# Performance work log

Hardware: AMD Instinct MI355X
Metric: run time of the kernel (lower is better)

## Reference

```python
import jax, jax.numpy as jnp
import numpy as np

TAU = 2.0        # LIF membrane time constant
VTH = 1.0        # firing threshold
ALPHA = 2.0      # ATan surrogate sharpness (spikingjelly default)
EPS = 1e-5       # LayerNorm eps


@jax.custom_vjp
def spike(x):
    # Heaviside forward, ATan surrogate backward (spikingjelly surrogate.ATan)
    return (x >= 0).astype(x.dtype)

def _spike_fwd(x):
    return (x >= 0).astype(x.dtype), x

def _spike_bwd(x, g):
    return (g * (ALPHA / 2.0) / (1.0 + (jnp.pi / 2.0 * ALPHA * x) ** 2),)

spike.defvjp(_spike_fwd, _spike_bwd)


def lif(x_tbd):
    """Multi-step LIF neuron, decay_input=True, hard reset v_reset=0, detach_reset=True.
    x_tbd: [T, B, D] -> spikes [T, B, D]."""
    def step(v, x):
        v = v + (x - v) / TAU                       # leaky integrate
        s = spike(v - VTH)                          # fire
        v = v * (1.0 - jax.lax.stop_gradient(s))    # detached hard reset to 0
        return v, s
    v0 = jnp.zeros(x_tbd.shape[1:], x_tbd.dtype)
    _, s = jax.lax.scan(step, v0, x_tbd)
    return s


def layernorm(x, g, b):
    m = x.mean(-1, keepdims=True)
    v = ((x - m) ** 2).mean(-1, keepdims=True)
    return (x - m) * jax.lax.rsqrt(v + EPS) * g + b


def setup_inputs() -> dict:
    key = jax.random.key(0)
    ks = jax.random.split(key, 8)
    B, T, IN, H0, D, HD, DEPTH = 64, 2048, 4, 64, 128, 256, 4
    def w(k, shape, fan_in):
        return jax.random.normal(k, shape, jnp.float32) * (1.0 / np.sqrt(fan_in))
    return {
        "hist_feat": jax.random.normal(ks[0], (B, T, IN), jnp.float32),
        # projector params
        "pw1": w(ks[1], (IN, H0), IN), "pb1": jnp.zeros((H0,), jnp.float32),
        "pw2": w(ks[2], (H0, D), H0), "pb2": jnp.zeros((D,), jnp.float32),
        # stacked block params [DEPTH, ...]
        "fc1_w": w(ks[3], (DEPTH, D, HD), D), "fc1_b": jnp.zeros((DEPTH, HD), jnp.float32),
        "n1_g": jnp.ones((DEPTH, HD), jnp.float32), "n1_b": jnp.zeros((DEPTH, HD), jnp.float32),
        "fc2_w": w(ks[4], (DEPTH, HD, D), HD), "fc2_b": jnp.zeros((DEPTH, D), jnp.float32),
        "n2_g": jnp.ones((DEPTH, D), jnp.float32), "n2_b": jnp.zeros((DEPTH, D), jnp.float32),
    }


def reference(hist_feat, pw1, pb1, pw2, pb2, fc1_w, fc1_b, n1_g, n1_b,
              fc2_w, fc2_b, n2_g, n2_b):
    # SpikeInputProjector: Linear -> exact GELU -> Linear
    x = jax.nn.gelu(hist_feat @ pw1 + pb1, approximate=False) @ pw2 + pb2  # [B,T,D]
    depth = fc1_w.shape[0]
    for i in range(depth):  # small fixed structural loop over blocks
        r = x
        h = layernorm(x @ fc1_w[i] + fc1_b[i], n1_g[i], n1_b[i])   # [B,T,HD]
        h = lif(h.swapaxes(0, 1)).swapaxes(0, 1)                    # LIF over time
        h = layernorm(h @ fc2_w[i] + fc2_b[i], n2_g[i], n2_b[i])   # [B,T,D]
        h = lif(h.swapaxes(0, 1)).swapaxes(0, 1)
        x = r + h
    return x[:, -1]  # pooling='last', mask=None
```

## Files before the change

### kernel.cpp

```cpp
#include <hip/hip_runtime.h>
#include <math.h>

#define NB   64
#define TT   2048
#define TW   64
#define T0   (TT - TW)
#define NR   (NB * TW)

typedef float v2f __attribute__((ext_vector_type(2)));

__device__ __forceinline__ float gelu_exact(float x) {
    return 0.5f * x * (1.0f + erff(x * 0.7071067811865476f));
}

#define XT_O   0
#define WB0_O  4096
#define WB1_O  20480
#define V1_O   36864
#define V2_O   37120
#define LB_TOT 37248

__global__ void __launch_bounds__(512) fused_kernel(
    const float* __restrict__ hist,
    const float* __restrict__ pw1, const float* __restrict__ pb1,
    const float* __restrict__ pw2, const float* __restrict__ pb2,
    const float* __restrict__ fc1w, const float* __restrict__ fc1b,
    const float* __restrict__ n1g,  const float* __restrict__ n1b,
    const float* __restrict__ fc2w, const float* __restrict__ fc2b,
    const float* __restrict__ n2g,  const float* __restrict__ n2b,
    float* __restrict__ v1buf, float* __restrict__ v2buf,
    int* __restrict__ flg1, int* __restrict__ flg2,
    float* __restrict__ out)
{
    __shared__ __align__(16) float LB[LB_TOT];
    __shared__ int FLG[2];
    const int tid = threadIdx.x, wave = tid >> 6, lane = tid & 63;
    const int b = blockIdx.x & 63, half = blockIdx.x >> 6;
    const int row0 = wave * 4;

    if (tid == 0) { FLG[0] = 0; FLG[1] = 0; }

    float4 r0, r1, r2, r3, r4, r5, r6, r7;
#define LOADQ(src) { const float4* p_ = (const float4*)(src); \
                     r0 = p_[tid];        r1 = p_[tid + 512]; \
                     r2 = p_[tid + 1024]; r3 = p_[tid + 1536]; \
                     r4 = p_[tid + 2048]; r5 = p_[tid + 2560]; \
                     r6 = p_[tid + 3072]; r7 = p_[tid + 3584]; }
#define WRITEQ(off) { float4* q_ = (float4*)&LB[off]; \
                      q_[tid]        = r0; q_[tid + 512]  = r1; \
                      q_[tid + 1024] = r2; q_[tid + 1536] = r3; \
                      q_[tid + 2048] = r4; q_[tid + 2560] = r5; \
                      q_[tid + 3072] = r6; q_[tid + 3584] = r7; }
#define CONSUME(WOFF, KQ) \
    { \
        _Pragma("unroll 2") \
        for (int k4 = 0; k4 < 16; ++k4) { \
            float4 xr[4]; \
            _Pragma("unroll") \
            for (int r = 0; r < 4; ++r) \
                xr[r] = *(const float4*)&LB[XT_O + (row0+r)*128 + (KQ) + k4*4]; \
            _Pragma("unroll") \
            for (int kk = 0; kk < 4; ++kk) { \
                float4 wv = ((const float4*)&LB[(WOFF) + (k4*4+kk)*256])[lane]; \
                v2f wA, wB; wA.x = wv.x; wA.y = wv.y; wB.x = wv.z; wB.y = wv.w; \
                _Pragma("unroll") \
                for (int r = 0; r < 4; ++r) { \
                    float xv = ((const float*)&xr[r])[kk]; \
                    accA[r] += wA * xv; \
                    accB[r] += wB * xv; \
                } \
            } \
        } \
    }

    LOADQ(fc1w);

    {
        const float* hb = hist + ((size_t)b * TT + T0 + half*32) * 4;
        float w0 = pw1[lane], w1 = pw1[64+lane], w2 = pw1[128+lane], w3 = pw1[192+lane];
        float bb = pb1[lane];
        #pragma unroll
        for (int r = 0; r < 4; ++r) {
            int t = row0 + r;
            float4 h = *(const float4*)(hb + t*4);
            LB[WB1_O + t*64 + lane] = gelu_exact(bb + h.x*w0 + h.y*w1 + h.z*w2 + h.w*w3);
        }
    }
    WRITEQ(WB0_O);
    LOADQ(fc1w + 16384);
    {
        float2 bv = ((const float2*)pb2)[lane];
        v2f acc[4];
        #pragma unroll
        for (int r = 0; r < 4; ++r) { acc[r].x = 0.f; acc[r].y = 0.f; }
        #pragma unroll 2
        for (int k4 = 0; k4 < 16; ++k4) {
            float4 xr[4];
            #pragma unroll
            for (int r = 0; r < 4; ++r)
                xr[r] = *(const float4*)&LB[WB1_O + (row0+r)*64 + k4*4];
            #pragma unroll
            for (int kk = 0; kk < 4; ++kk) {
                v2f w = ((const v2f*)(pw2 + (k4*4+kk)*128))[lane];
                #pragma unroll
                for (int r = 0; r < 4; ++r) {
                    float xv = ((const float*)&xr[r])[kk];
                    acc[r] += w * xv;
                }
            }
        }
        #pragma unroll
        for (int r = 0; r < 4; ++r) {
            float2 o; o.x = acc[r].x + bv.x; o.y = acc[r].y + bv.y;
            *(float2*)&LB[XT_O + (row0+r)*128 + lane*2] = o;
        }
    }

    #pragma unroll 1
    for (int l = 0; l < 4; ++l) {
        const float* W1n = fc1w + (size_t)(l < 3 ? l+1 : l) * 32768;
        const float* W2g = fc2w + (size_t)l * 32768;

        v2f accA[4], accB[4];
        #pragma unroll
        for (int r = 0; r < 4; ++r) {
            accA[r].x = 0.f; accA[r].y = 0.f;
            accB[r].x = 0.f; accB[r].y = 0.f;
        }
        __syncthreads(); WRITEQ(WB1_O); LOADQ(W1n);          CONSUME(WB0_O, 0);
        __syncthreads(); WRITEQ(WB0_O); LOADQ(W1n + 16384);  CONSUME(WB1_O, 64);

        {
            float4 b1v = ((const float4*)(fc1b + l*256))[lane];
            float4 g1v = ((const float4*)(n1g  + l*256))[lane];
            float4 t1v = ((const float4*)(n1b  + l*256))[lane];
            #pragma unroll
            for (int r = 0; r < 4; ++r) {
                float a0 = accA[r].x + b1v.x, a1 = accA[r].y + b1v.y;
                float a2 = accB[r].x + b1v.z, a3 = accB[r].y + b1v.w;
                float s = a0 + a1 + a2 + a3;
                #pragma unroll
                for (int m = 1; m < 64; m <<= 1) s += __shfl_xor(s, m, 64);
                float mean = s * (1.0f/256.0f);
                float dx = a0-mean, dy = a1-mean, dz = a2-mean, dw = a3-mean;
                float q2 = dx*dx + dy*dy + dz*dz + dw*dw;
                #pragma unroll
                for (int m = 1; m < 64; m <<= 1) q2 += __shfl_xor(q2, m, 64);
                float inv = 1.0f / sqrtf(q2 * (1.0f/256.0f) + 1e-5f);
                accA[r].x = dx*inv*g1v.x + t1v.x; accA[r].y = dy*inv*g1v.y + t1v.y;
                accB[r].x = dz*inv*g1v.z + t1v.z; accB[r].y = dw*inv*g1v.w + t1v.w;
            }
        }
        unsigned long long Mk[4][4];
        {
            const int tgt = l*8 + wave;
            while (__hip_atomic_load(&FLG[0], __ATOMIC_ACQUIRE,
                                     __HIP_MEMORY_SCOPE_WORKGROUP) < tgt)
                __builtin_amdgcn_s_sleep(1);
            float v0, v1, v2, v3;
            if (wave == 0) {
                if (half == 0) { v0 = v1 = v2 = v3 = 0.f; }
                else {
                    while (__hip_atomic_load(&flg1[b], __ATOMIC_RELAXED,
                                             __HIP_MEMORY_SCOPE_AGENT) < l+1)
                        __builtin_amdgcn_s_sleep(1);
                    __builtin_amdgcn_fence(__ATOMIC_ACQUIRE, "agent");
                    float4 vv = *(const float4*)&v1buf[(size_t)l*NB*256 + b*256 + lane*4];
                    v0 = vv.x; v1 = vv.y; v2 = vv.z; v3 = vv.w;
                }
            } else {
                float4 vv = *(const float4*)&LB[V1_O + lane*4];
                v0 = vv.x; v1 = vv.y; v2 = vv.z; v3 = vv.w;
            }
            #pragma unroll
            for (int i = 0; i < 4; ++i) {
                v0 += (accA[i].x - v0) * 0.5f;
                v1 += (accA[i].y - v1) * 0.5f;
                v2 += (accB[i].x - v2) * 0.5f;
                v3 += (accB[i].y - v3) * 0.5f;
                bool s0 = v0 >= 1.f, s1 = v1 >= 1.f, s2 = v2 >= 1.f, s3 = v3 >= 1.f;
                Mk[0][i] = __ballot(s0); Mk[1][i] = __ballot(s1);
                Mk[2][i] = __ballot(s2); Mk[3][i] = __ballot(s3);
                v0 = s0 ? 0.f : v0;  v1 = s1 ? 0.f : v1;
                v2 = s2 ? 0.f : v2;  v3 = s3 ? 0.f : v3;
            }
            if (wave < 7) {
                float4 vv; vv.x = v0; vv.y = v1; vv.z = v2; vv.w = v3;
                *(float4*)&LB[V1_O + lane*4] = vv;
            } else if (half == 0) {
                float4 vv; vv.x = v0; vv.y = v1; vv.z = v2; vv.w = v3;
                *(float4*)&v1buf[(size_t)l*NB*256 + b*256 + lane*4] = vv;
                __builtin_amdgcn_fence(__ATOMIC_RELEASE, "agent");
                if (lane == 0)
                    __hip_atomic_store(&flg1[b], l+1, __ATOMIC_RELAXED,
                                       __HIP_MEMORY_SCOPE_AGENT);
            }
            if (lane == 0)
                __hip_atomic_store(&FLG[0], tgt+1, __ATOMIC_RELEASE,
                                   __HIP_MEMORY_SCOPE_WORKGROUP);
        }
        float a2x[4], a2y[4];
        #pragma unroll
        for (int i = 0; i < 4; ++i) {
            unsigned long long m0 = Mk[0][i], m1 = Mk[1][i];
            unsigned long long m2 = Mk[2][i], m3 = Mk[3][i];
            unsigned long long mm = m0 | m1 | m2 | m3;
            float ax = 0.f, ay = 0.f;
            int ng = __popcll(mm) >> 2;
            for (int g = 0; g < ng; ++g) {
                int i0 = __builtin_ctzll(mm); mm &= mm - 1;
                int i1 = __builtin_ctzll(mm); mm &= mm - 1;
                int i2 = __builtin_ctzll(mm); mm &= mm - 1;
                int i3 = __builtin_ctzll(mm); mm &= mm - 1;
                const float* p0 = W2g + (size_t)i0 * 512;
                const float* p1 = W2g + (size_t)i1 * 512;
                const float* p2 = W2g + (size_t)i2 * 512;
                const float* p3 = W2g + (size_t)i3 * 512;
                float2 w00 = ((const float2*)(p0      ))[lane];
                float2 w01 = ((const float2*)(p0 + 128))[lane];
                float2 w02 = ((const float2*)(p0 + 256))[lane];
                float2 w03 = ((const float2*)(p0 + 384))[lane];
                float2 w10 = ((const float2*)(p1      ))[lane];
                float2 w11 = ((const float2*)(p1 + 128))[lane];
                float2 w12 = ((const float2*)(p1 + 256))[lane];
                float2 w13 = ((const float2*)(p1 + 384))[lane];
                float2 w20 = ((const float2*)(p2      ))[lane];
                float2 w21 = ((const float2*)(p2 + 128))[lane];
                float2 w22 = ((const float2*)(p2 + 256))[lane];
                float2 w23 = ((const float2*)(p2 + 384))[lane];
                float2 w30 = ((const float2*)(p3      ))[lane];
                float2 w31 = ((const float2*)(p3 + 128))[lane];
                float2 w32 = ((const float2*)(p3 + 256))[lane];
                float2 w33 = ((const float2*)(p3 + 384))[lane];
                unsigned long long b0 = 1ull << i0, b1 = 1ull << i1;
                unsigned long long b2 = 1ull << i2, b3 = 1ull << i3;
                ax += (m0 & b0) ? w00.x : 0.f;  ay += (m0 & b0) ? w00.y : 0.f;
                ax += (m1 & b0) ? w01.x : 0.f;  ay += (m1 & b0) ? w01.y : 0.f;
                ax += (m2 & b0) ? w02.x : 0.f;  ay += (m2 & b0) ? w02.y : 0.f;
                ax += (m3 & b0) ? w03.x : 0.f;  ay += (m3 & b0) ? w03.y : 0.f;
                ax += (m0 & b1) ? w10.x : 0.f;  ay += (m0 & b1) ? w10.y : 0.f;
                ax += (m1 & b1) ? w11.x : 0.f;  ay += (m1 & b1) ? w11.y : 0.f;
                ax += (m2 & b1) ? w12.x : 0.f;  ay += (m2 & b1) ? w12.y : 0.f;
                ax += (m3 & b1) ? w13.x : 0.f;  ay += (m3 & b1) ? w13.y : 0.f;
                ax += (m0 & b2) ? w20.x : 0.f;  ay += (m0 & b2) ? w20.y : 0.f;
                ax += (m1 & b2) ? w21.x : 0.f;  ay += (m1 & b2) ? w21.y : 0.f;
                ax += (m2 & b2) ? w22.x : 0.f;  ay += (m2 & b2) ? w22.y : 0.f;
                ax += (m3 & b2) ? w23.x : 0.f;  ay += (m3 & b2) ? w23.y : 0.f;
                ax += (m0 & b3) ? w30.x : 0.f;  ay += (m0 & b3) ? w30.y : 0.f;
                ax += (m1 & b3) ? w31.x : 0.f;  ay += (m1 & b3) ? w31.y : 0.f;
                ax += (m2 & b3) ? w32.x : 0.f;  ay += (m2 & b3) ? w32.y : 0.f;
                ax += (m3 & b3) ? w33.x : 0.f;  ay += (m3 & b3) ? w33.y : 0.f;
            }
            while (mm) {
                int id = __builtin_ctzll(mm); mm &= mm - 1;
                const float* wr = W2g + (size_t)id * 512;
                float2 w0 = ((const float2*)(wr      ))[lane];
                float2 w1 = ((const float2*)(wr + 128))[lane];
                float2 w2 = ((const float2*)(wr + 256))[lane];
                float2 w3 = ((const float2*)(wr + 384))[lane];
                unsigned long long bit = 1ull << id;
                ax += (m0 & bit) ? w0.x : 0.f;  ay += (m0 & bit) ? w0.y : 0.f;
                ax += (m1 & bit) ? w1.x : 0.f;  ay += (m1 & bit) ? w1.y : 0.f;
                ax += (m2 & bit) ? w2.x : 0.f;  ay += (m2 & bit) ? w2.y : 0.f;
                ax += (m3 & bit) ? w3.x : 0.f;  ay += (m3 & bit) ? w3.y : 0.f;
            }
            a2x[i] = ax; a2y[i] = ay;
        }
        {
            float2 b2v = ((const float2*)(fc2b + l*128))[lane];
            float2 g2v = ((const float2*)(n2g  + l*128))[lane];
            float2 t2v = ((const float2*)(n2b  + l*128))[lane];
            #pragma unroll
            for (int i = 0; i < 4; ++i) {
                float ax = a2x[i] + b2v.x, ay = a2y[i] + b2v.y;
                float s = ax + ay;
                #pragma unroll
                for (int m = 1; m < 64; m <<= 1) s += __shfl_xor(s, m, 64);
                float mean = s * (1.0f/128.0f);
                float dx = ax - mean, dy = ay - mean;
                float q = dx*dx + dy*dy;
                #pragma unroll
                for (int m = 1; m < 64; m <<= 1) q += __shfl_xor(q, m, 64);
                float inv = 1.0f / sqrtf(q * (1.0f/128.0f) + 1e-5f);
                a2x[i] = dx*inv*g2v.x + t2v.x;
                a2y[i] = dy*inv*g2v.y + t2v.y;
            }
        }
        {
            const int tgt = l*8 + wave;
            while (__hip_atomic_load(&FLG[1], __ATOMIC_ACQUIRE,
                                     __HIP_MEMORY_SCOPE_WORKGROUP) < tgt)
                __builtin_amdgcn_s_sleep(1);
            float u0, u1;
            if (wave == 0) {
                if (half == 0) { u0 = u1 = 0.f; }
                else {
                    while (__hip_atomic_load(&flg2[b], __ATOMIC_RELAXED,
                                             __HIP_MEMORY_SCOPE_AGENT) < l+1)
                        __builtin_amdgcn_s_sleep(1);
                    __builtin_amdgcn_fence(__ATOMIC_ACQUIRE, "agent");
                    float2 uv = *(const float2*)&v2buf[(size_t)l*NB*128 + b*128 + lane*2];
                    u0 = uv.x; u1 = uv.y;
                }
            } else {
                float2 uv = *(const float2*)&LB[V2_O + lane*2];
                u0 = uv.x; u1 = uv.y;
            }
            #pragma unroll
            for (int i = 0; i < 4; ++i) {
                int t = row0 + i;
                u0 += (a2x[i] - u0) * 0.5f;
                u1 += (a2y[i] - u1) * 0.5f;
                bool s0 = u0 >= 1.f, s1 = u1 >= 1.f;
                float2 xv = *(const float2*)&LB[XT_O + t*128 + lane*2];
                float2 xn;
                xn.x = xv.x + (s0 ? 1.f : 0.f);
                xn.y = xv.y + (s1 ? 1.f : 0.f);
                *(float2*)&LB[XT_O + t*128 + lane*2] = xn;
                u0 = s0 ? 0.f : u0;
                u1 = s1 ? 0.f : u1;
                if (l == 3 && half == 1 && t == 31)
                    ((float2*)(out + b*128))[lane] = xn;
            }
            if (wave < 7) {
                float2 uv; uv.x = u0; uv.y = u1;
                *(float2*)&LB[V2_O + lane*2] = uv;
            } else if (half == 0) {
                float2 uv; uv.x = u0; uv.y = u1;
                *(float2*)&v2buf[(size_t)l*NB*128 + b*128 + lane*2] = uv;
                __builtin_amdgcn_fence(__ATOMIC_RELEASE, "agent");
                if (lane == 0)
                    __hip_atomic_store(&flg2[b], l+1, __ATOMIC_RELAXED,
                                       __HIP_MEMORY_SCOPE_AGENT);
            }
            if (lane == 0)
                __hip_atomic_store(&FLG[1], tgt+1, __ATOMIC_RELEASE,
                                   __HIP_MEMORY_SCOPE_WORKGROUP);
        }
    }
#undef LOADQ
#undef WRITEQ
#undef CONSUME
}

extern "C" void kernel_launch(void* const* d_in, const int* in_sizes, int n_in,
                              void* d_out, int out_size, void* d_ws, size_t ws_size,
                              hipStream_t stream) {
    const float* hist = (const float*)d_in[0];
    const float* pw1  = (const float*)d_in[1];
    const float* pb1  = (const float*)d_in[2];
    const float* pw2  = (const float*)d_in[3];
    const float* pb2  = (const float*)d_in[4];
    const float* fc1w = (const float*)d_in[5];
    const float* fc1b = (const float*)d_in[6];
    const float* n1g  = (const float*)d_in[7];
    const float* n1b  = (const float*)d_in[8];
    const float* fc2w = (const float*)d_in[9];
    const float* fc2b = (const float*)d_in[10];
    const float* n2g  = (const float*)d_in[11];
    const float* n2b  = (const float*)d_in[12];
    float* out = (float*)d_out;

    char* ws = (char*)d_ws;
    float* v1buf = (float*)ws;
    float* v2buf = (float*)(ws + (1ull << 20));
    int*   flg1  = (int*)(ws + (2ull << 20));
    int*   flg2  = flg1 + 64;

    hipMemsetAsync(flg1, 0, 128 * sizeof(int), stream);
    fused_kernel<<<128, 512, 0, stream>>>(hist, pw1, pb1, pw2, pb2,
                                          fc1w, fc1b, n1g, n1b,
                                          fc2w, fc2b, n2g, n2b,
                                          v1buf, v2buf, flg1, flg2, out);
}
```

Measured before the change: 182.5 us.

## Split the time window across four blocks per batch with chained LIF state handoff

Each batch's 64-step window is now split across four workgroups of 16 timesteps each instead of two of 32, so the grid doubles to 256 blocks and each wave handles 2 rows instead of 4. LIF membrane state is passed down a chain of three inter-block handoffs through global buffers and per-quarter flags. The goal is to use more CUs and shrink each block's matmul work. The cost is a longer serial dependency chain between blocks, more global flag spinning, and every block reloading the full weights, which adds memory traffic.

```diff
diff --git a/kernel.cpp b/kernel.cpp
--- a/kernel.cpp
+++ b/kernel.cpp
@@ -14,11 +14,11 @@
 }
 
 #define XT_O   0
-#define WB0_O  4096
-#define WB1_O  20480
-#define V1_O   36864
-#define V2_O   37120
-#define LB_TOT 37248
+#define WB0_O  2048
+#define WB1_O  18432
+#define V1_O   34816
+#define V2_O   35072
+#define LB_TOT 35200
 
 __global__ void __launch_bounds__(512) fused_kernel(
     const float* __restrict__ hist,
@@ -35,8 +35,8 @@
     __shared__ __align__(16) float LB[LB_TOT];
     __shared__ int FLG[2];
     const int tid = threadIdx.x, wave = tid >> 6, lane = tid & 63;
-    const int b = blockIdx.x & 63, half = blockIdx.x >> 6;
-    const int row0 = wave * 4;
+    const int b = blockIdx.x & 63, q = blockIdx.x >> 6;
+    const int row0 = wave * 2;
 
     if (tid == 0) { FLG[0] = 0; FLG[1] = 0; }
 
@@ -55,16 +55,16 @@
     { \
         _Pragma("unroll 2") \
         for (int k4 = 0; k4 < 16; ++k4) { \
-            float4 xr[4]; \
+            float4 xr[2]; \
             _Pragma("unroll") \
-            for (int r = 0; r < 4; ++r) \
+            for (int r = 0; r < 2; ++r) \
                 xr[r] = *(const float4*)&LB[XT_O + (row0+r)*128 + (KQ) + k4*4]; \
             _Pragma("unroll") \
             for (int kk = 0; kk < 4; ++kk) { \
                 float4 wv = ((const float4*)&LB[(WOFF) + (k4*4+kk)*256])[lane]; \
                 v2f wA, wB; wA.x = wv.x; wA.y = wv.y; wB.x = wv.z; wB.y = wv.w; \
                 _Pragma("unroll") \
-                for (int r = 0; r < 4; ++r) { \
+                for (int r = 0; r < 2; ++r) { \
                     float xv = ((const float*)&xr[r])[kk]; \
                     accA[r] += wA * xv; \
                     accB[r] += wB * xv; \
@@ -76,11 +76,11 @@
     LOADQ(fc1w);
 
     {
-        const float* hb = hist + ((size_t)b * TT + T0 + half*32) * 4;
+        const float* hb = hist + ((size_t)b * TT + T0 + q*16) * 4;
         float w0 = pw1[lane], w1 = pw1[64+lane], w2 = pw1[128+lane], w3 = pw1[192+lane];
         float bb = pb1[lane];
         #pragma unroll
-        for (int r = 0; r < 4; ++r) {
+        for (int r = 0; r < 2; ++r) {
             int t = row0 + r;
             float4 h = *(const float4*)(hb + t*4);
             LB[WB1_O + t*64 + lane] = gelu_exact(bb + h.x*w0 + h.y*w1 + h.z*w2 + h.w*w3);
@@ -90,27 +90,27 @@
     LOADQ(fc1w + 16384);
     {
         float2 bv = ((const float2*)pb2)[lane];
-        v2f acc[4];
-        #pragma unroll
-        for (int r = 0; r < 4; ++r) { acc[r].x = 0.f; acc[r].y = 0.f; }
+        v2f acc[2];
+        #pragma unroll
+        for (int r = 0; r < 2; ++r) { acc[r].x = 0.f; acc[r].y = 0.f; }
         #pragma unroll 2
         for (int k4 = 0; k4 < 16; ++k4) {
-            float4 xr[4];
-            #pragma unroll
-            for (int r = 0; r < 4; ++r)
+            float4 xr[2];
+            #pragma unroll
+            for (int r = 0; r < 2; ++r)
                 xr[r] = *(const float4*)&LB[WB1_O + (row0+r)*64 + k4*4];
             #pragma unroll
             for (int kk = 0; kk < 4; ++kk) {
                 v2f w = ((const v2f*)(pw2 + (k4*4+kk)*128))[lane];
                 #pragma unroll
-                for (int r = 0; r < 4; ++r) {
+                for (int r = 0; r < 2; ++r) {
                     float xv = ((const float*)&xr[r])[kk];
                     acc[r] += w * xv;
                 }
             }
         }
         #pragma unroll
-        for (int r = 0; r < 4; ++r) {
+        for (int r = 0; r < 2; ++r) {
             float2 o; o.x = acc[r].x + bv.x; o.y = acc[r].y + bv.y;
             *(float2*)&LB[XT_O + (row0+r)*128 + lane*2] = o;
         }
@@ -121,9 +121,9 @@
         const float* W1n = fc1w + (size_t)(l < 3 ? l+1 : l) * 32768;
         const float* W2g = fc2w + (size_t)l * 32768;
 
-        v2f accA[4], accB[4];
-        #pragma unroll
-        for (int r = 0; r < 4; ++r) {
+        v2f accA[2], accB[2];
+        #pragma unroll
+        for (int r = 0; r < 2; ++r) {
             accA[r].x = 0.f; accA[r].y = 0.f;
             accB[r].x = 0.f; accB[r].y = 0.f;
         }
@@ -135,7 +135,7 @@
             float4 g1v = ((const float4*)(n1g  + l*256))[lane];
             float4 t1v = ((const float4*)(n1b  + l*256))[lane];
             #pragma unroll
-            for (int r = 0; r < 4; ++r) {
+            for (int r = 0; r < 2; ++r) {
                 float a0 = accA[r].x + b1v.x, a1 = accA[r].y + b1v.y;
                 float a2 = accB[r].x + b1v.z, a3 = accB[r].y + b1v.w;
                 float s = a0 + a1 + a2 + a3;
@@ -151,7 +151,7 @@
                 accB[r].x = dz*inv*g1v.z + t1v.z; accB[r].y = dw*inv*g1v.w + t1v.w;
             }
         }
-        unsigned long long Mk[4][4];
+        unsigned long long Mk[4][2];
         {
             const int tgt = l*8 + wave;
             while (__hip_atomic_load(&FLG[0], __ATOMIC_ACQUIRE,
@@ -159,13 +159,14 @@
                 __builtin_amdgcn_s_sleep(1);
             float v0, v1, v2, v3;
             if (wave == 0) {
-                if (half == 0) { v0 = v1 = v2 = v3 = 0.f; }
+                if (q == 0) { v0 = v1 = v2 = v3 = 0.f; }
                 else {
-                    while (__hip_atomic_load(&flg1[b], __ATOMIC_RELAXED,
+                    while (__hip_atomic_load(&flg1[(q-1)*64 + b], __ATOMIC_RELAXED,
                                              __HIP_MEMORY_SCOPE_AGENT) < l+1)
                         __builtin_amdgcn_s_sleep(1);
                     __builtin_amdgcn_fence(__ATOMIC_ACQUIRE, "agent");
-                    float4 vv = *(const float4*)&v1buf[(size_t)l*NB*256 + b*256 + lane*4];
+                    float4 vv = *(const float4*)
+                        &v1buf[(size_t)(l*3 + (q-1))*NB*256 + b*256 + lane*4];
                     v0 = vv.x; v1 = vv.y; v2 = vv.z; v3 = vv.w;
                 }
             } else {
@@ -173,7 +174,7 @@
                 v0 = vv.x; v1 = vv.y; v2 = vv.z; v3 = vv.w;
             }
             #pragma unroll
-            for (int i = 0; i < 4; ++i) {
+            for (int i = 0; i < 2; ++i) {
                 v0 += (accA[i].x - v0) * 0.5f;
                 v1 += (accA[i].y - v1) * 0.5f;
                 v2 += (accB[i].x - v2) * 0.5f;
@@ -187,21 +188,21 @@
             if (wave < 7) {
                 float4 vv; vv.x = v0; vv.y = v1; vv.z = v2; vv.w = v3;
                 *(float4*)&LB[V1_O + lane*4] = vv;
-            } else if (half == 0) {
+            } else if (q < 3) {
                 float4 vv; vv.x = v0; vv.y = v1; vv.z = v2; vv.w = v3;
-                *(float4*)&v1buf[(size_t)l*NB*256 + b*256 + lane*4] = vv;
+                *(float4*)&v1buf[(size_t)(l*3 + q)*NB*256 + b*256 + lane*4] = vv;
                 __builtin_amdgcn_fence(__ATOMIC_RELEASE, "agent");
                 if (lane == 0)
-                    __hip_atomic_store(&flg1[b], l+1, __ATOMIC_RELAXED,
+                    __hip_atomic_store(&flg1[q*64 + b], l+1, __ATOMIC_RELAXED,
                                        __HIP_MEMORY_SCOPE_AGENT);
             }
             if (lane == 0)
                 __hip_atomic_store(&FLG[0], tgt+1, __ATOMIC_RELEASE,
                                    __HIP_MEMORY_SCOPE_WORKGROUP);
         }
-        float a2x[4], a2y[4];
-        #pragma unroll
-        for (int i = 0; i < 4; ++i) {
+        float a2x[2], a2y[2];
+        #pragma unroll
+        for (int i = 0; i < 2; ++i) {
             unsigned long long m0 = Mk[0][i], m1 = Mk[1][i];
             unsigned long long m2 = Mk[2][i], m3 = Mk[3][i];
             unsigned long long mm = m0 | m1 | m2 | m3;
@@ -271,17 +272,17 @@
             float2 g2v = ((const float2*)(n2g  + l*128))[lane];
             float2 t2v = ((const float2*)(n2b  + l*128))[lane];
             #pragma unroll
-            for (int i = 0; i < 4; ++i) {
+            for (int i = 0; i < 2; ++i) {
                 float ax = a2x[i] + b2v.x, ay = a2y[i] + b2v.y;
                 float s = ax + ay;
                 #pragma unroll
                 for (int m = 1; m < 64; m <<= 1) s += __shfl_xor(s, m, 64);
                 float mean = s * (1.0f/128.0f);
                 float dx = ax - mean, dy = ay - mean;
-                float q = dx*dx + dy*dy;
-                #pragma unroll
-                for (int m = 1; m < 64; m <<= 1) q += __shfl_xor(q, m, 64);
-                float inv = 1.0f / sqrtf(q * (1.0f/128.0f) + 1e-5f);
+                float qq = dx*dx + dy*dy;
+                #pragma unroll
+                for (int m = 1; m < 64; m <<= 1) qq += __shfl_xor(qq, m, 64);
+                float inv = 1.0f / sqrtf(qq * (1.0f/128.0f) + 1e-5f);
                 a2x[i] = dx*inv*g2v.x + t2v.x;
                 a2y[i] = dy*inv*g2v.y + t2v.y;
             }
@@ -293,13 +294,14 @@
                 __builtin_amdgcn_s_sleep(1);
             float u0, u1;
             if (wave == 0) {
-                if (half == 0) { u0 = u1 = 0.f; }
+                if (q == 0) { u0 = u1 = 0.f; }
                 else {
-                    while (__hip_atomic_load(&flg2[b], __ATOMIC_RELAXED,
+                    while (__hip_atomic_load(&flg2[(q-1)*64 + b], __ATOMIC_RELAXED,
                                              __HIP_MEMORY_SCOPE_AGENT) < l+1)
                         __builtin_amdgcn_s_sleep(1);
                     __builtin_amdgcn_fence(__ATOMIC_ACQUIRE, "agent");
-                    float2 uv = *(const float2*)&v2buf[(size_t)l*NB*128 + b*128 + lane*2];
+                    float2 uv = *(const float2*)
+                        &v2buf[(size_t)(l*3 + (q-1))*NB*128 + b*128 + lane*2];
                     u0 = uv.x; u1 = uv.y;
                 }
             } else {
@@ -307,7 +309,7 @@
                 u0 = uv.x; u1 = uv.y;
             }
             #pragma unroll
-            for (int i = 0; i < 4; ++i) {
+            for (int i = 0; i < 2; ++i) {
                 int t = row0 + i;
                 u0 += (a2x[i] - u0) * 0.5f;
                 u1 += (a2y[i] - u1) * 0.5f;
@@ -319,18 +321,18 @@
                 *(float2*)&LB[XT_O + t*128 + lane*2] = xn;
                 u0 = s0 ? 0.f : u0;
                 u1 = s1 ? 0.f : u1;
-                if (l == 3 && half == 1 && t == 31)
+                if (l == 3 && q == 3 && t == 15)
                     ((float2*)(out + b*128))[lane] = xn;
             }
             if (wave < 7) {
                 float2 uv; uv.x = u0; uv.y = u1;
                 *(float2*)&LB[V2_O + lane*2] = uv;
-            } else if (half == 0) {
+            } else if (q < 3) {
                 float2 uv; uv.x = u0; uv.y = u1;
-                *(float2*)&v2buf[(size_t)l*NB*128 + b*128 + lane*2] = uv;
+                *(float2*)&v2buf[(size_t)(l*3 + q)*NB*128 + b*128 + lane*2] = uv;
                 __builtin_amdgcn_fence(__ATOMIC_RELEASE, "agent");
                 if (lane == 0)
-                    __hip_atomic_store(&flg2[b], l+1, __ATOMIC_RELAXED,
+                    __hip_atomic_store(&flg2[q*64 + b], l+1, __ATOMIC_RELAXED,
                                        __HIP_MEMORY_SCOPE_AGENT);
             }
             if (lane == 0)
@@ -365,10 +367,10 @@
     float* v1buf = (float*)ws;
     float* v2buf = (float*)(ws + (1ull << 20));
     int*   flg1  = (int*)(ws + (2ull << 20));
-    int*   flg2  = flg1 + 64;
-
-    hipMemsetAsync(flg1, 0, 128 * sizeof(int), stream);
-    fused_kernel<<<128, 512, 0, stream>>>(hist, pw1, pb1, pw2, pb2,
+    int*   flg2  = flg1 + 256;
+
+    hipMemsetAsync(flg1, 0, 512 * sizeof(int), stream);
+    fused_kernel<<<256, 512, 0, stream>>>(hist, pw1, pb1, pw2, pb2,
                                           fc1w, fc1b, n1g, n1b,
                                           fc2w, fc2b, n2g, n2b,
                                           v1buf, v2buf, flg1, flg2, out);
```

After: 177.6 us, median of 2. 1.03x faster.
